# Kernel optimization log

Hardware: AMD Instinct MI355X
Metric: run time of the kernel (lower is better)

The kernel has to match this reference:

```python
import jax, jax.numpy as jnp
import numpy as np

U, I, E, D, R = 100000, 50000, 2000000, 64, 5


def setup_inputs() -> dict:
    key = jax.random.key(0)
    ks = jax.random.split(key, 14)
    def n(k, shape, scale=0.05):
        return jax.random.normal(k, shape, jnp.float32) * scale
    return {
        "user_feat": n(ks[0], (U, D), 1.0),
        "item_feat": n(ks[1], (I, D), 1.0),
        "rating_feat": n(ks[2], (R, D), 1.0),
        "row_idxs": jax.random.randint(ks[3], (E,), 0, I),   # item index per edge
        "col_idxs": jax.random.randint(ks[4], (E,), 0, U),   # user index per edge (dst)
        "rating": jax.random.randint(ks[5], (E,), 0, R),
        # gv = Linear(2D,D)+ReLU -> Linear(D,D)+ReLU
        "gv_w1": n(ks[6], (2 * D, D)), "gv_b1": jnp.zeros((D,), jnp.float32),
        "gv_w2": n(ks[7], (D, D)),     "gv_b2": jnp.zeros((D,), jnp.float32),
        # Attention: Linear(2D,D)+ReLU -> Linear(D,D)+ReLU -> Linear(D,1)
        "att_w1": n(ks[8], (2 * D, D)), "att_b1": jnp.zeros((D,), jnp.float32),
        "att_w2": n(ks[9], (D, D)),     "att_b2": jnp.zeros((D,), jnp.float32),
        "att_w3": n(ks[10], (D, 1)),    "att_b3": jnp.zeros((1,), jnp.float32),
        # output projection w = Linear(D,D)
        "w_w": n(ks[11], (D, D)), "w_b": jnp.zeros((D,), jnp.float32),
    }


def segment_softmax(logits, seg, num_segments):
    # numerically stable softmax over edges grouped by destination node
    m = jax.ops.segment_max(logits, seg, num_segments=num_segments)
    e = jnp.exp(logits - m[seg])
    s = jax.ops.segment_sum(e, seg, num_segments=num_segments)
    return e / s[seg]


def reference(user_feat, item_feat, rating_feat, row_idxs, col_idxs, rating,
              gv_w1, gv_b1, gv_w2, gv_b2,
              att_w1, att_b1, att_w2, att_b2, att_w3, att_b3,
              w_w, w_b):
    # gather per-edge embeddings
    r_emb = rating_feat[rating]          # [E, D]
    i_emb = item_feat[row_idxs]          # [E, D]
    u_emb = user_feat[col_idxs]          # [E, D]
    # gv MLP on concat(item, rating)
    x = jnp.concatenate([i_emb, r_emb], axis=1)              # [E, 2D]
    h1 = jax.nn.relu(x @ gv_w1 + gv_b1)
    x_ia = jax.nn.relu(h1 @ gv_w2 + gv_b2)                   # [E, D]
    # attention MLP on concat(x_ia, user)
    a = jnp.concatenate([x_ia, u_emb], axis=1)               # [E, 2D]
    a = jax.nn.relu(a @ att_w1 + att_b1)
    a = jax.nn.relu(a @ att_w2 + att_b2)
    weight = (a @ att_w3 + att_b3)[:, 0]                     # [E]
    # edge_softmax over incoming edges of each destination (user) node
    value = segment_softmax(weight, col_idxs, U)             # [E]
    # scatter-sum weighted messages to users
    h = jax.ops.segment_sum(x_ia * value[:, None], col_idxs, num_segments=U)  # [U, D]
    # act is None -> plain linear
    return h @ w_w + w_b
```

## Files before the change

### kernel.cpp

```cpp
#include <hip/hip_runtime.h>
#include <hip/hip_bf16.h>
#include <hip/hip_fp8.h>

#define U_N 100000
#define I_N 50000
#define E_N 2000000
#define R_N 5
#define C_N (I_N*R_N)
#define NBLK_U 391
#define NBLK_E 7813
#define NBLK_C 1954
#define NBUCKC 196

typedef __hip_bfloat16 bf16_t;
typedef unsigned short u16;
typedef unsigned char u8;
typedef __attribute__((ext_vector_type(8))) short bf16x8;
typedef __attribute__((ext_vector_type(4))) float f32x4;

__device__ __forceinline__ float blo(unsigned u){ return __uint_as_float(u<<16); }
__device__ __forceinline__ float bhi(unsigned u){ return __uint_as_float(u & 0xffff0000u); }
__device__ __forceinline__ unsigned pkbf(float a, float b){
  __hip_bfloat162 t = __float22bfloat162_rn(float2{a,b});
  union { __hip_bfloat162 h; unsigned u; } cv; cv.h = t; return cv.u;
}
__device__ __forceinline__ u16 f2b(float v){
  union { __hip_bfloat16 h; u16 u; } cv; cv.h = __float2bfloat16(v); return cv.u;
}
__device__ __forceinline__ float f8f(unsigned b){
  __hip_fp8_e4m3 h; h.__x = (u8)b; return (float)h;
}
__device__ __forceinline__ unsigned ff8(float f){
  __hip_fp8_e4m3 h(f); return (unsigned)h.__x;
}

__global__ __launch_bounds__(256) void k_histQ(const int* __restrict__ cols, int* __restrict__ hist_g){
  __shared__ int histI[NBUCKC];
  int t = threadIdx.x, b = blockIdx.x;
  if(t < NBUCKC) histI[t] = 0;
  __syncthreads();
  int e = b*256 + t;
  if(e < E_N) atomicAdd(&histI[cols[e] >> 9], 1);
  __syncthreads();
  if(t < NBUCKC) hist_g[(size_t)b*NBUCKC + t] = histI[t];
}

__global__ __launch_bounds__(256) void k_scanQ(const int* __restrict__ hist_g, int* __restrict__ boff_g,
                                               int* __restrict__ qtot){
  __shared__ int wsum[4];
  int t = threadIdx.x, q = blockIdx.x;
  int lane = t & 63, wv = t >> 6;
  int running = 0;
  for(int c0=0; c0<NBLK_E; c0+=256){
    int b = c0 + t;
    int v = (b < NBLK_E) ? hist_g[(size_t)b*NBUCKC + q] : 0;
    int inc = v;
#pragma unroll
    for(int off=1; off<64; off<<=1){
      int x = __shfl(inc, lane-off);
      if(lane >= off) inc += x;
    }
    if(lane == 63) wsum[wv] = inc;
    __syncthreads();
    int w0=wsum[0], w1=wsum[1], w2=wsum[2], w3=wsum[3];
    int wpre = (wv>0?w0:0) + (wv>1?w1:0) + (wv>2?w2:0);
    if(b < NBLK_E) boff_g[(size_t)b*NBUCKC + q] = running + wpre + inc - v;
    running += w0 + w1 + w2 + w3;
    __syncthreads();
  }
  if(t == 0) qtot[q] = running;
}

__global__ void k_scanT(const int* __restrict__ qtot, int* __restrict__ qbase){
  __shared__ int s[256];
  int t = threadIdx.x;
  int v = (t < NBUCKC) ? qtot[t] : 0;
  s[t] = v; __syncthreads();
  for(int off=1; off<256; off<<=1){
    int x = (t>=off) ? s[t-off] : 0;
    __syncthreads();
    s[t] += x;
    __syncthreads();
  }
  if(t < NBUCKC) qbase[t] = s[t] - v;
  if(t == 255)   qbase[NBUCKC] = s[255];
}

__global__ __launch_bounds__(256) void k_place2(const int* __restrict__ rows, const int* __restrict__ cols,
                                                const int* __restrict__ rats,
                                                const int* __restrict__ boff_g, const int* __restrict__ qbase,
                                                unsigned* __restrict__ uc2){
  __shared__ int rankI[NBUCKC];
  __shared__ int baseI[NBUCKC];
  int t = threadIdx.x, b = blockIdx.x;
  if(t < NBUCKC){
    rankI[t] = 0;
    baseI[t] = qbase[t] + boff_g[(size_t)b*NBUCKC + t];
  }
  __syncthreads();
  int e = b*256 + t;
  if(e < E_N){
    int u = cols[e];
    int c = rows[e]*5 + rats[e];
    int q = u >> 9;
    int r = atomicAdd(&rankI[q], 1);
    uc2[baseI[q] + r] = ((unsigned)(u & 511) << 18) | (unsigned)c;
  }
}

__global__ __launch_bounds__(256) void k_fineB1(const unsigned* __restrict__ uc2, const int* __restrict__ qbase,
                                                int* __restrict__ cnt){
  __shared__ int hist[512];
  int t = threadIdx.x, q = blockIdx.x;
  hist[t] = 0; hist[t+256] = 0;
  __syncthreads();
  int r0 = qbase[q], r1 = qbase[q+1];
  for(int j=r0+t; j<r1; j+=256) atomicAdd(&hist[(uc2[j]>>18) & 511], 1);
  __syncthreads();
  cnt[q*512 + t]       = hist[t];
  cnt[q*512 + t + 256] = hist[t+256];
}

__global__ __launch_bounds__(256) void k_scanA(const int* __restrict__ cnt, int* __restrict__ start,
                                               int* __restrict__ bsum){
  __shared__ int s[256];
  int t = threadIdx.x, i = blockIdx.x*256 + t;
  int v = (i < U_N) ? cnt[i] : 0;
  s[t] = v; __syncthreads();
  for(int off=1; off<256; off<<=1){
    int x = (t>=off) ? s[t-off] : 0;
    __syncthreads();
    s[t] += x;
    __syncthreads();
  }
  start[i] = s[t] - v;
  if(t == 255) bsum[blockIdx.x] = s[255];
}

__global__ void k_scanB(int* bsum, int n){
  __shared__ int s[512];
  int t = threadIdx.x;
  int v = (t < n) ? bsum[t] : 0;
  s[t] = v; __syncthreads();
  for(int off=1; off<512; off<<=1){
    int x = (t>=off) ? s[t-off] : 0;
    __syncthreads();
    s[t] += x;
    __syncthreads();
  }
  if(t < n) bsum[t] = s[t] - v;
}

__global__ __launch_bounds__(256) void k_scanC(int* start, const int* __restrict__ bsum){
  int i = blockIdx.x*256 + threadIdx.x;
  start[i] += bsum[blockIdx.x];
}

__global__ __launch_bounds__(256) void k_fineB2(const unsigned* __restrict__ uc2, const int* __restrict__ qbase,
                                                const int* __restrict__ start,
                                                int* __restrict__ u_s, int* __restrict__ c_s){
  __shared__ int fillb[512];
  __shared__ int startb[512];
  int t = threadIdx.x, q = blockIdx.x;
  fillb[t] = 0; fillb[t+256] = 0;
  startb[t]     = start[q*512 + t];
  startb[t+256] = start[q*512 + t + 256];
  __syncthreads();
  int r0 = qbase[q], r1 = qbase[q+1];
  for(int j=r0+t; j<r1; j+=256){
    unsigned v = uc2[j];
    int ul = (int)((v>>18) & 511);
    int off = atomicAdd(&fillb[ul], 1);
    int pos = startb[ul] + off;
    u_s[pos] = (q<<9) | ul;
    c_s[pos] = (int)(v & 0x3FFFFu);
  }
}

__global__ void k_ratpart(const float* __restrict__ rf, const float* __restrict__ w1,
                          const float* __restrict__ b1, float* __restrict__ out){
  int t = threadIdx.x; if(t >= R_N*64) return;
  int r = t>>6, d = t&63;
  float acc = b1[d];
  for(int k=0;k<64;k++) acc += rf[r*64 + k] * w1[(64+k)*64 + d];
  out[t] = acc;
}

__global__ __launch_bounds__(256) void k_prepw6(const float* __restrict__ w1, const float* __restrict__ a1,
                                                const float* __restrict__ w2, const float* __restrict__ a2,
                                                const float* __restrict__ ww,
                                                u16* w1t, u16* u1t, u16* w2t, u16* a1t, u16* a2t, u16* wwt){
  int idx = (blockIdx.x & 15)*256 + threadIdx.x;
  int sec = blockIdx.x >> 4;
  int d = idx >> 6, k = idx & 63;
  const float* src; u16* dst; int ko = 0;
  switch(sec){
    case 0: src=w1; dst=w1t; break;
    case 1: src=a1; dst=u1t; ko=64; break;
    case 2: src=w2; dst=w2t; break;
    case 3: src=a1; dst=a1t; break;
    case 4: src=a2; dst=a2t; break;
    default: src=ww; dst=wwt; break;
  }
  dst[idx] = f2b(src[(size_t)(ko+k)*64 + d]);
}

template<bool BIAS>
__global__ __launch_bounds__(256) void k_rowgemm(const float4* __restrict__ in,
                                                 const uint4* __restrict__ wt,
                                                 const float* __restrict__ bias,
                                                 uint4* __restrict__ outp, int n){
  __shared__ uint4 A_u4[2048];
  __shared__ uint4 W_u4[512];
  __shared__ float bsh[64];
  u16* A16 = (u16*)A_u4;
  const int tid = threadIdx.x;
  for(int cid = tid; cid < 512; cid += 256){
    int dd = cid >> 3, ch = cid & 7;
    W_u4[dd*8 + (ch ^ (dd&7))] = wt[cid];
  }
  if(BIAS && tid < 64) bsh[tid] = bias[tid];
  const int base = blockIdx.x*256;
  const int ch = tid & 7;
#pragma unroll
  for(int it=0; it<8; ++it){
    int s = it*32 + (tid>>3);
    int r = base + s;
    uint4 o = {0,0,0,0};
    if(r < n){
      const float4* p = in + (size_t)r*16 + ch*2;
      float4 v0 = p[0], v1 = p[1];
      o.x = pkbf(v0.x, v0.y); o.y = pkbf(v0.z, v0.w);
      o.z = pkbf(v1.x, v1.y); o.w = pkbf(v1.z, v1.w);
    }
    A_u4[s*8 + (ch ^ (s&7))] = o;
  }
  __syncthreads();
  const int l = tid & 63, w = tid >> 6;
  const int lr = l & 15, g = l >> 4;
  bf16x8 bfr[4][2];
#pragma unroll
  for(int nt=0; nt<4; ++nt)
#pragma unroll
    for(int kk=0; kk<2; ++kk){
      int d = nt*16 + lr;
      bfr[nt][kk] = *(const bf16x8*)&W_u4[d*8 + ((kk*4+g) ^ (d&7))];
    }
  float bv[4];
#pragma unroll
  for(int nt=0; nt<4; ++nt) bv[nt] = BIAS ? bsh[nt*16 + lr] : 0.f;
#pragma unroll
  for(int t=0; t<4; ++t){
    int s = w*64 + t*16 + lr;
    bf16x8 af0 = *(const bf16x8*)&A_u4[s*8 + ((0*4+g) ^ (s&7))];
    bf16x8 af1 = *(const bf16x8*)&A_u4[s*8 + ((1*4+g) ^ (s&7))];
    f32x4 acc[4];
#pragma unroll
    for(int nt=0; nt<4; ++nt){
      f32x4 c0 = { bv[nt], bv[nt], bv[nt], bv[nt] };
      c0 = __builtin_amdgcn_mfma_f32_16x16x32_bf16(af0, bfr[nt][0], c0, 0, 0, 0);
      c0 = __builtin_amdgcn_mfma_f32_16x16x32_bf16(af1, bfr[nt][1], c0, 0, 0, 0);
      acc[nt] = c0;
    }
#pragma unroll
    for(int nt=0; nt<4; ++nt){
      int d = nt*16 + lr;
#pragma unroll
      for(int reg=0; reg<4; ++reg){
        int srow = w*64 + t*16 + g*4 + reg;
        A16[srow*64 + ((d>>3)^(srow&7))*8 + (d&7)] = f2b(acc[nt][reg]);
      }
    }
  }
#pragma unroll
  for(int it=0; it<8; ++it){
    int s = w*64 + it*8 + (l>>3);
    int c2 = l & 7;
    int r = base + s;
    if(r < n) outp[(size_t)r*8 + c2] = A_u4[s*8 + (c2 ^ (s&7))];
  }
}

__global__ __launch_bounds__(256) void k_combo_mfma(const uint4* __restrict__ itemp,
                                                    const float4* __restrict__ ratp,
                                                    const uint4* __restrict__ w2t_g, const uint4* __restrict__ a1t_g,
                                                    const uint4* __restrict__ wwt_g,
                                                    const float* __restrict__ b2,
                                                    uint4* __restrict__ y_o, u8* __restrict__ xa1_o8){
  __shared__ uint4 A_u4[1024];
  __shared__ uint4 X_u4[1024];
  __shared__ uint4 W2_u4[512];
  __shared__ uint4 A1_u4[512];
  __shared__ uint4 WW_u4[512];
  __shared__ float4 rsh4[80];
  __shared__ float b2sh[64];
  u16* A16 = (u16*)A_u4;
  u16* X16 = (u16*)X_u4;
  const int tid = threadIdx.x;
  for(int cid = tid; cid < 512; cid += 256){
    int dd = cid >> 3, ch = cid & 7;
    W2_u4[dd*8 + (ch ^ (dd&7))] = w2t_g[cid];
    A1_u4[dd*8 + (ch ^ (dd&7))] = a1t_g[cid];
    WW_u4[dd*8 + (ch ^ (dd&7))] = wwt_g[cid];
  }
  if(tid < 80) rsh4[tid] = ratp[tid];
  if(tid < 64) b2sh[tid] = b2[tid];
  __syncthreads();

  const int base = blockIdx.x*128;
  const int ch = tid & 7;
#pragma unroll
  for(int it=0; it<4; ++it){
    int s = it*32 + (tid>>3);
    int cidx = base + s;
    uint4 o = {0,0,0,0};
    if(cidx < C_N){
      int i = cidx/5, r = cidx - i*5;
      uint4 iv = itemp[(size_t)i*8 + ch];
      float4 r0 = rsh4[r*16 + ch*2], r1 = rsh4[r*16 + ch*2 + 1];
      o.x = pkbf(fmaxf(blo(iv.x)+r0.x,0.f), fmaxf(bhi(iv.x)+r0.y,0.f));
      o.y = pkbf(fmaxf(blo(iv.y)+r0.z,0.f), fmaxf(bhi(iv.y)+r0.w,0.f));
      o.z = pkbf(fmaxf(blo(iv.z)+r1.x,0.f), fmaxf(bhi(iv.z)+r1.y,0.f));
      o.w = pkbf(fmaxf(blo(iv.w)+r1.z,0.f), fmaxf(bhi(iv.w)+r1.w,0.f));
    }
    A_u4[s*8 + (ch ^ (s&7))] = o;
  }
  __syncthreads();

  const int l = tid & 63, w = tid >> 6;
  const int lr = l & 15, g = l >> 4;
  bf16x8 w2f[4][2], a1f[4][2], wwf[4][2];
#pragma unroll
  for(int nt=0; nt<4; ++nt)
#pragma unroll
    for(int kk=0; kk<2; ++kk){
      int d = nt*16 + lr;
      w2f[nt][kk] = *(const bf16x8*)&W2_u4[d*8 + ((kk*4+g) ^ (d&7))];
      a1f[nt][kk] = *(const bf16x8*)&A1_u4[d*8 + ((kk*4+g) ^ (d&7))];
      wwf[nt][kk] = *(const bf16x8*)&WW_u4[d*8 + ((kk*4+g) ^ (d&7))];
    }
  float b2v[4];
#pragma unroll
  for(int nt=0; nt<4; ++nt) b2v[nt] = b2sh[nt*16 + lr];

#pragma unroll
  for(int t=0; t<2; ++t){
    int s = w*32 + t*16 + lr;
    bf16x8 af0 = *(const bf16x8*)&A_u4[s*8 + ((0*4+g) ^ (s&7))];
    bf16x8 af1 = *(const bf16x8*)&A_u4[s*8 + ((1*4+g) ^ (s&7))];
#pragma unroll
    for(int nt=0; nt<4; ++nt){
      f32x4 c0 = { b2v[nt], b2v[nt], b2v[nt], b2v[nt] };
      c0 = __builtin_amdgcn_mfma_f32_16x16x32_bf16(af0, w2f[nt][0], c0, 0, 0, 0);
      c0 = __builtin_amdgcn_mfma_f32_16x16x32_bf16(af1, w2f[nt][1], c0, 0, 0, 0);
      int d = nt*16 + lr;
#pragma unroll
      for(int reg=0; reg<4; ++reg){
        int srow = w*32 + t*16 + g*4 + reg;
        X16[srow*64 + ((d>>3)^(srow&7))*8 + (d&7)] = f2b(fmaxf(c0[reg], 0.f));
      }
    }
    bf16x8 xf0 = *(const bf16x8*)&X_u4[s*8 + ((0*4+g) ^ (s&7))];
    bf16x8 xf1 = *(const bf16x8*)&X_u4[s*8 + ((1*4+g) ^ (s&7))];
#pragma unroll
    for(int nt=0; nt<4; ++nt){
      f32x4 c0 = { 0.f, 0.f, 0.f, 0.f };
      c0 = __builtin_amdgcn_mfma_f32_16x16x32_bf16(xf0, a1f[nt][0], c0, 0, 0, 0);
      c0 = __builtin_amdgcn_mfma_f32_16x16x32_bf16(xf1, a1f[nt][1], c0, 0, 0, 0);
      int d = nt*16 + lr;
#pragma unroll
      for(int reg=0; reg<4; ++reg){
        int srow = w*32 + t*16 + g*4 + reg;
        A16[srow*64 + ((d>>3)^(srow&7))*8 + (d&7)] = f2b(c0[reg]);
      }
    }
#pragma unroll
    for(int nt=0; nt<4; ++nt){
      f32x4 c0 = { 0.f, 0.f, 0.f, 0.f };
      c0 = __builtin_amdgcn_mfma_f32_16x16x32_bf16(xf0, wwf[nt][0], c0, 0, 0, 0);
      c0 = __builtin_amdgcn_mfma_f32_16x16x32_bf16(xf1, wwf[nt][1], c0, 0, 0, 0);
      int d = nt*16 + lr;
#pragma unroll
      for(int reg=0; reg<4; ++reg){
        int srow = w*32 + t*16 + g*4 + reg;
        X16[srow*64 + ((d>>3)^(srow&7))*8 + (d&7)] = f2b(c0[reg]);
      }
    }
  }
#pragma unroll
  for(int it=0; it<4; ++it){
    int s = w*32 + it*8 + (l>>3);
    int c2 = l & 7;
    int r = base + s;
    if(r < C_N) y_o[(size_t)r*8 + c2] = X_u4[s*8 + (c2 ^ (s&7))];
  }
#pragma unroll
  for(int it=0; it<2; ++it){
    int slot = it*64 + l;
    int rl = slot >> 2;
    int c4 = slot & 3;
    int s = w*32 + rl;
    int r = base + s;
    if(r < C_N){
      uint4 h0 = A_u4[s*8 + ((c4*2+0) ^ (s&7))];
      uint4 h1 = A_u4[s*8 + ((c4*2+1) ^ (s&7))];
      uint4 o;
      o.x = ff8(blo(h0.x)) | (ff8(bhi(h0.x))<<8) | (ff8(blo(h0.y))<<16) | (ff8(bhi(h0.y))<<24);
      o.y = ff8(blo(h0.z)) | (ff8(bhi(h0.z))<<8) | (ff8(blo(h0.w))<<16) | (ff8(bhi(h0.w))<<24);
      o.z = ff8(blo(h1.x)) | (ff8(bhi(h1.x))<<8) | (ff8(blo(h1.y))<<16) | (ff8(bhi(h1.y))<<24);
      o.w = ff8(blo(h1.z)) | (ff8(bhi(h1.z))<<8) | (ff8(blo(h1.w))<<16) | (ff8(bhi(h1.w))<<24);
      *(uint4*)(xa1_o8 + (size_t)r*64 + c4*16) = o;
    }
  }
}

__global__ __launch_bounds__(256) void k_edge_mfma(const int* __restrict__ u_s, const int* __restrict__ c_s,
                                                   const u8* __restrict__ xa1p8, const uint4* __restrict__ userp,
                                                   const u16* __restrict__ w2t_g,
                                                   const float* __restrict__ a2b,
                                                   const float* __restrict__ a3w, const float* __restrict__ a3b,
                                                   float* __restrict__ wlog){
  const int tid = threadIdx.x;
  const int base = blockIdx.x*256;
  const int l = tid & 63, w = tid >> 6;
  const int lr = l & 15;
  const int g  = l >> 4;
  bf16x8 bf[4][2];
#pragma unroll
  for(int nt=0; nt<4; ++nt)
#pragma unroll
    for(int kk=0; kk<2; ++kk){
      int d = nt*16 + lr;
      bf[nt][kk] = *(const bf16x8*)(w2t_g + d*64 + kk*32 + g*8);
    }
  float b2v[4], a3v[4];
#pragma unroll
  for(int nt=0; nt<4; ++nt){ b2v[nt] = a2b[nt*16 + lr]; a3v[nt] = a3w[nt*16 + lr]; }
  const float a3b0 = a3b[0];

  int cin[4], uin[4];
#pragma unroll
  for(int t=0; t<4; ++t){
    int s = base + w*64 + t*16 + lr;
    cin[t] = (s < E_N) ? c_s[s] : 0;
    uin[t] = (s < E_N) ? u_s[s] : 0;
  }
  uint2 xq0 = *(const uint2*)(xa1p8 + (size_t)cin[0]*64 + g*8);
  uint2 xq1 = *(const uint2*)(xa1p8 + (size_t)cin[0]*64 + 32 + g*8);
  uint4 uv0 = userp[(size_t)uin[0]*8 + g];
  uint4 uv1 = userp[(size_t)uin[0]*8 + 4 + g];

#pragma unroll
  for(int t=0; t<4; ++t){
    uint2 nx0, nx1; uint4 nu0, nu1;
    if(t < 3){
      nx0 = *(const uint2*)(xa1p8 + (size_t)cin[t+1]*64 + g*8);
      nx1 = *(const uint2*)(xa1p8 + (size_t)cin[t+1]*64 + 32 + g*8);
      nu0 = userp[(size_t)uin[t+1]*8 + g];
      nu1 = userp[(size_t)uin[t+1]*8 + 4 + g];
    }
    union { uint4 u4; bf16x8 v; } a0, a1;
    a0.u4.x = pkbf(fmaxf(f8f(xq0.x&255u)+blo(uv0.x),0.f),       fmaxf(f8f((xq0.x>>8)&255u)+bhi(uv0.x),0.f));
    a0.u4.y = pkbf(fmaxf(f8f((xq0.x>>16)&255u)+blo(uv0.y),0.f), fmaxf(f8f(xq0.x>>24)+bhi(uv0.y),0.f));
    a0.u4.z = pkbf(fmaxf(f8f(xq0.y&255u)+blo(uv0.z),0.f),       fmaxf(f8f((xq0.y>>8)&255u)+bhi(uv0.z),0.f));
    a0.u4.w = pkbf(fmaxf(f8f((xq0.y>>16)&255u)+blo(uv0.w),0.f), fmaxf(f8f(xq0.y>>24)+bhi(uv0.w),0.f));
    a1.u4.x = pkbf(fmaxf(f8f(xq1.x&255u)+blo(uv1.x),0.f),       fmaxf(f8f((xq1.x>>8)&255u)+bhi(uv1.x),0.f));
    a1.u4.y = pkbf(fmaxf(f8f((xq1.x>>16)&255u)+blo(uv1.y),0.f), fmaxf(f8f(xq1.x>>24)+bhi(uv1.y),0.f));
    a1.u4.z = pkbf(fmaxf(f8f(xq1.y&255u)+blo(uv1.z),0.f),       fmaxf(f8f((xq1.y>>8)&255u)+bhi(uv1.z),0.f));
    a1.u4.w = pkbf(fmaxf(f8f((xq1.y>>16)&255u)+blo(uv1.w),0.f), fmaxf(f8f(xq1.y>>24)+bhi(uv1.w),0.f));
    f32x4 acc[4];
#pragma unroll
    for(int nt=0; nt<4; ++nt){
      f32x4 c0 = { b2v[nt], b2v[nt], b2v[nt], b2v[nt] };
      c0 = __builtin_amdgcn_mfma_f32_16x16x32_bf16(a0.v, bf[nt][0], c0, 0, 0, 0);
      c0 = __builtin_amdgcn_mfma_f32_16x16x32_bf16(a1.v, bf[nt][1], c0, 0, 0, 0);
      acc[nt] = c0;
    }
    float s0=0.f, s1=0.f, s2=0.f, s3=0.f;
#pragma unroll
    for(int nt=0; nt<4; ++nt){
      s0 += fmaxf(acc[nt][0], 0.f) * a3v[nt];
      s1 += fmaxf(acc[nt][1], 0.f) * a3v[nt];
      s2 += fmaxf(acc[nt][2], 0.f) * a3v[nt];
      s3 += fmaxf(acc[nt][3], 0.f) * a3v[nt];
    }
#pragma unroll
    for(int mask=1; mask<16; mask<<=1){
      s0 += __shfl_xor(s0, mask);
      s1 += __shfl_xor(s1, mask);
      s2 += __shfl_xor(s2, mask);
      s3 += __shfl_xor(s3, mask);
    }
    if(lr == 0){
      int e0 = base + w*64 + t*16 + g*4;
      if(e0+0 < E_N) wlog[e0+0] = s0 + a3b0;
      if(e0+1 < E_N) wlog[e0+1] = s1 + a3b0;
      if(e0+2 < E_N) wlog[e0+2] = s2 + a3b0;
      if(e0+3 < E_N) wlog[e0+3] = s3 + a3b0;
    }
    xq0 = nx0; xq1 = nx1; uv0 = nu0; uv1 = nu1;
  }
}

__global__ __launch_bounds__(256) void k_aggf(const int* __restrict__ start,
                                              const int* __restrict__ u_s, const int* __restrict__ c_s,
                                              const float* __restrict__ wlog,
                                              const u16* __restrict__ Y,
                                              const float* __restrict__ wb,
                                              float* __restrict__ out){
  __shared__ uint4 Ysh[4][256];
  int w = threadIdx.x >> 6, l = threadIdx.x & 63;
  int lr = l & 15, g = l >> 4;
  int base = (blockIdx.x*4 + w) * 16;
  if(base >= U_N) return;
  int s0g = start[base];
  int s1g = start[base+16];
  int myu = base + lr;
  int sA = s0g & ~31;
  int nch = (s1g - sA + 31) >> 5;
  const int kb = g*8;

  float m = -1e30f;
  for(int ch=0; ch<nch; ++ch){
    int e0 = sA + ch*32;
    float4 wv0 = *(const float4*)(wlog + e0 + kb);
    float4 wv1 = *(const float4*)(wlog + e0 + kb + 4);
    int4 u0 = *(const int4*)(u_s + e0 + kb);
    int4 u1 = *(const int4*)(u_s + e0 + kb + 4);
    if(u0.x==myu) m = fmaxf(m, wv0.x);
    if(u0.y==myu) m = fmaxf(m, wv0.y);
    if(u0.z==myu) m = fmaxf(m, wv0.z);
    if(u0.w==myu) m = fmaxf(m, wv0.w);
    if(u1.x==myu) m = fmaxf(m, wv1.x);
    if(u1.y==myu) m = fmaxf(m, wv1.y);
    if(u1.z==myu) m = fmaxf(m, wv1.z);
    if(u1.w==myu) m = fmaxf(m, wv1.w);
  }
  m = fmaxf(m, __shfl_xor(m, 16));
  m = fmaxf(m, __shfl_xor(m, 32));

  f32x4 acc[4];
#pragma unroll
  for(int nt=0; nt<4; ++nt) acc[nt] = f32x4{0.f,0.f,0.f,0.f};
  float ssum = 0.f;
  u16* Ysh16 = (u16*)&Ysh[w][0];
  for(int ch=0; ch<nch; ++ch){
    int e0 = sA + ch*32;
    int rowe = e0 + (l>>1);
    int crow = c_s[rowe];
    const uint4* yp = (const uint4*)Y + (size_t)crow*8 + (l&1)*4;
    uint4* dst = &Ysh[w][(l>>1)*8 + (l&1)*4];
    dst[0] = yp[0]; dst[1] = yp[1]; dst[2] = yp[2]; dst[3] = yp[3];

    float4 wv0 = *(const float4*)(wlog + e0 + kb);
    float4 wv1 = *(const float4*)(wlog + e0 + kb + 4);
    int4 u0 = *(const int4*)(u_s + e0 + kb);
    int4 u1 = *(const int4*)(u_s + e0 + kb + 4);
    bf16x8 af;
    {
      bool mt; float e;
      mt = (u0.x==myu); e = __expf((mt?wv0.x:-1e30f) - m); ssum += mt?e:0.f; af[0] = mt?(short)f2b(e):(short)0;
      mt = (u0.y==myu); e = __expf((mt?wv0.y:-1e30f) - m); ssum += mt?e:0.f; af[1] = mt?(short)f2b(e):(short)0;
      mt = (u0.z==myu); e = __expf((mt?wv0.z:-1e30f) - m); ssum += mt?e:0.f; af[2] = mt?(short)f2b(e):(short)0;
      mt = (u0.w==myu); e = __expf((mt?wv0.w:-1e30f) - m); ssum += mt?e:0.f; af[3] = mt?(short)f2b(e):(short)0;
      mt = (u1.x==myu); e = __expf((mt?wv1.x:-1e30f) - m); ssum += mt?e:0.f; af[4] = mt?(short)f2b(e):(short)0;
      mt = (u1.y==myu); e = __expf((mt?wv1.y:-1e30f) - m); ssum += mt?e:0.f; af[5] = mt?(short)f2b(e):(short)0;
      mt = (u1.z==myu); e = __expf((mt?wv1.z:-1e30f) - m); ssum += mt?e:0.f; af[6] = mt?(short)f2b(e):(short)0;
      mt = (u1.w==myu); e = __expf((mt?wv1.w:-1e30f) - m); ssum += mt?e:0.f; af[7] = mt?(short)f2b(e):(short)0;
    }
    bf16x8 b0, b1, b2, b3;
#pragma unroll
    for(int j=0; j<8; ++j){
      int r = (kb + j)*64 + lr;
      b0[j] = (short)Ysh16[r];
      b1[j] = (short)Ysh16[r+16];
      b2[j] = (short)Ysh16[r+32];
      b3[j] = (short)Ysh16[r+48];
    }
    acc[0] = __builtin_amdgcn_mfma_f32_16x16x32_bf16(af, b0, acc[0], 0, 0, 0);
    acc[1] = __builtin_amdgcn_mfma_f32_16x16x32_bf16(af, b1, acc[1], 0, 0, 0);
    acc[2] = __builtin_amdgcn_mfma_f32_16x16x32_bf16(af, b2, acc[2], 0, 0, 0);
    acc[3] = __builtin_amdgcn_mfma_f32_16x16x32_bf16(af, b3, acc[3], 0, 0, 0);
  }
  ssum += __shfl_xor(ssum, 16);
  ssum += __shfl_xor(ssum, 32);
  float inv = (ssum > 0.f) ? (1.f/ssum) : 0.f;
  float wbv[4];
#pragma unroll
  for(int nt=0; nt<4; ++nt) wbv[nt] = wb[nt*16 + lr];
#pragma unroll
  for(int reg=0; reg<4; ++reg){
    float sc = __shfl(inv, g*4 + reg);
    int u = base + g*4 + reg;
#pragma unroll
    for(int nt=0; nt<4; ++nt)
      out[(size_t)u*64 + nt*16 + lr] = acc[nt][reg]*sc + wbv[nt];
  }
}

extern "C" void kernel_launch(void* const* d_in, const int* in_sizes, int n_in,
                              void* d_out, int out_size, void* d_ws, size_t ws_size,
                              hipStream_t stream){
  (void)in_sizes; (void)n_in; (void)out_size; (void)ws_size;
  const float4* user_feat  = (const float4*)d_in[0];
  const float4* item_feat  = (const float4*)d_in[1];
  const float*  rating_feat= (const float*)d_in[2];
  const int*    rows       = (const int*)d_in[3];
  const int*    cols       = (const int*)d_in[4];
  const int*    rats       = (const int*)d_in[5];
  const float* gv_w1 = (const float*)d_in[6];
  const float* gv_b1 = (const float*)d_in[7];
  const float* gv_w2 = (const float*)d_in[8];
  const float* gv_b2 = (const float*)d_in[9];
  const float* att_w1= (const float*)d_in[10];
  const float* att_b1= (const float*)d_in[11];
  const float* att_w2= (const float*)d_in[12];
  const float* att_b2= (const float*)d_in[13];
  const float* att_w3= (const float*)d_in[14];
  const float* att_b3= (const float*)d_in[15];
  const float* w_w   = (const float*)d_in[16];
  const float* w_b   = (const float*)d_in[17];
  float* out = (float*)d_out;

  char* ws = (char*)d_ws; size_t off = 0;
  auto take = [&](size_t b)->char*{ char* p = ws + off; off = (off + b + 255) & ~(size_t)255; return p; };
  bf16_t*   item_part  = (bf16_t*)take((size_t)I_N*64*2);
  bf16_t*   user_part  = (bf16_t*)take((size_t)U_N*64*2);
  float*    rating_part= (float*) take((size_t)R_N*64*4);
  bf16_t*   y_t        = (bf16_t*)take((size_t)C_N*64*2);
  u8*       xa1_8      = (u8*)    take((size_t)C_N*64);
  float*    wlog_s     = (float*) take((size_t)E_N*4);
  int*      c_s        = (int*)   take((size_t)E_N*4);
  int*      u_s        = (int*)   take((size_t)E_N*4);
  unsigned* uc2        = (unsigned*)take((size_t)E_N*4);
  int*      hist_g     = (int*)   take((size_t)NBLK_E*NBUCKC*4);
  int*      boff_g     = (int*)   take((size_t)NBLK_E*NBUCKC*4);
  int*      qtot       = (int*)   take((size_t)256*4);
  int*      qbase      = (int*)   take((size_t)256*4);
  int*      cnt        = (int*)   take((size_t)(NBUCKC*512+256)*4);
  int*      start      = (int*)   take((size_t)(NBUCKC*512+256)*4);
  int*      bsum       = (int*)   take((size_t)512*4);
  u16*      w1t        = (u16*)   take((size_t)4096*2);
  u16*      u1t        = (u16*)   take((size_t)4096*2);
  u16*      w2t        = (u16*)   take((size_t)4096*2);
  u16*      a1t        = (u16*)   take((size_t)4096*2);
  u16*      a2t        = (u16*)   take((size_t)4096*2);
  u16*      wwt        = (u16*)   take((size_t)4096*2);

  k_histQ <<<NBLK_E, 256, 0, stream>>>(cols, hist_g);
  k_scanQ <<<NBUCKC, 256, 0, stream>>>(hist_g, boff_g, qtot);
  k_scanT <<<1, 256, 0, stream>>>(qtot, qbase);
  k_place2<<<NBLK_E, 256, 0, stream>>>(rows, cols, rats, boff_g, qbase, uc2);
  k_fineB1<<<NBUCKC, 256, 0, stream>>>(uc2, qbase, cnt);
  k_scanA <<<NBLK_U, 256, 0, stream>>>(cnt, start, bsum);
  k_scanB <<<1, 512, 0, stream>>>(bsum, NBLK_U);
  k_scanC <<<NBLK_U, 256, 0, stream>>>(start, bsum);
  k_fineB2<<<NBUCKC, 256, 0, stream>>>(uc2, qbase, start, u_s, c_s);
  k_ratpart <<<1, 320, 0, stream>>>(rating_feat, gv_w1, gv_b1, rating_part);
  k_prepw6  <<<96, 256, 0, stream>>>(gv_w1, att_w1, gv_w2, att_w2, w_w, w1t, u1t, w2t, a1t, a2t, wwt);
  k_rowgemm<false><<<(I_N+255)/256, 256, 0, stream>>>(item_feat, (const uint4*)w1t, nullptr,
                                                      (uint4*)item_part, I_N);
  k_rowgemm<true> <<<NBLK_U, 256, 0, stream>>>(user_feat, (const uint4*)u1t, att_b1,
                                               (uint4*)user_part, U_N);
  k_combo_mfma<<<NBLK_C, 256, 0, stream>>>((const uint4*)item_part, (const float4*)rating_part,
                                           (const uint4*)w2t, (const uint4*)a1t, (const uint4*)wwt, gv_b2,
                                           (uint4*)y_t, xa1_8);
  k_edge_mfma<<<NBLK_E, 256, 0, stream>>>(u_s, c_s, xa1_8, (const uint4*)user_part,
                                          w2t, att_b2, att_w3, att_b3, wlog_s);
  k_aggf <<<(U_N/64)+1, 256, 0, stream>>>(start, u_s, c_s, wlog_s, (const u16*)y_t, w_b, out);
}
```

Baseline: 310.5 us.

## Pack user/item indices into one sorted word and double-buffer aggregation loads

Replaces the separate sorted user and item index arrays with a single packed 32-bit array. It stores 14 bits of user id above an 18-bit combo id, which cuts index write and read traffic in the sort, edge and aggregation kernels. The edge kernel rebuilds the full user id from a per-block bucket lookup plus a short scan over bucket boundaries, and its gathers are restructured into a two-deep prefetch. The aggregation kernel double-buffers the gathered Y rows in shared memory so the next chunk's loads overlap the current MFMAs. The cost is an extra small kernel, more shared memory, and a per-edge while loop over bucket boundaries.

```diff
diff --git a/kernel.cpp b/kernel.cpp
--- a/kernel.cpp
+++ b/kernel.cpp
@@ -86,6 +86,14 @@
   if(t == 255)   qbase[NBUCKC] = s[255];
 }
 
+__global__ __launch_bounds__(256) void k_blockq(const int* __restrict__ qbase, int* __restrict__ blockq){
+  int b = blockIdx.x*256 + threadIdx.x; if(b >= NBLK_E) return;
+  int e = b*256;
+  int lo = 0, hi = NBUCKC-1;
+  while(lo < hi){ int mid = (lo+hi+1)>>1; if(qbase[mid] <= e) lo = mid; else hi = mid-1; }
+  blockq[b] = lo;
+}
+
 __global__ __launch_bounds__(256) void k_place2(const int* __restrict__ rows, const int* __restrict__ cols,
                                                 const int* __restrict__ rats,
                                                 const int* __restrict__ boff_g, const int* __restrict__ qbase,
@@ -104,7 +112,7 @@
     int c = rows[e]*5 + rats[e];
     int q = u >> 9;
     int r = atomicAdd(&rankI[q], 1);
-    uc2[baseI[q] + r] = ((unsigned)(u & 511) << 18) | (unsigned)c;
+    uc2[baseI[q] + r] = ((unsigned)(u & 16383) << 18) | (unsigned)c;
   }
 }
 
@@ -158,7 +166,7 @@
 
 __global__ __launch_bounds__(256) void k_fineB2(const unsigned* __restrict__ uc2, const int* __restrict__ qbase,
                                                 const int* __restrict__ start,
-                                                int* __restrict__ u_s, int* __restrict__ c_s){
+                                                unsigned* __restrict__ uc3){
   __shared__ int fillb[512];
   __shared__ int startb[512];
   int t = threadIdx.x, q = blockIdx.x;
@@ -171,9 +179,7 @@
     unsigned v = uc2[j];
     int ul = (int)((v>>18) & 511);
     int off = atomicAdd(&fillb[ul], 1);
-    int pos = startb[ul] + off;
-    u_s[pos] = (q<<9) | ul;
-    c_s[pos] = (int)(v & 0x3FFFFu);
+    uc3[startb[ul] + off] = v;
   }
 }
 
@@ -414,7 +420,8 @@
   }
 }
 
-__global__ __launch_bounds__(256) void k_edge_mfma(const int* __restrict__ u_s, const int* __restrict__ c_s,
+__global__ __launch_bounds__(256) void k_edge_mfma(const unsigned* __restrict__ uc3,
+                                                   const int* __restrict__ qbase, const int* __restrict__ blockq,
                                                    const u8* __restrict__ xa1p8, const uint4* __restrict__ userp,
                                                    const u16* __restrict__ w2t_g,
                                                    const float* __restrict__ a2b,
@@ -439,26 +446,19 @@
   const float a3b0 = a3b[0];
 
   int cin[4], uin[4];
+  int bq = blockq[blockIdx.x];
 #pragma unroll
   for(int t=0; t<4; ++t){
     int s = base + w*64 + t*16 + lr;
-    cin[t] = (s < E_N) ? c_s[s] : 0;
-    uin[t] = (s < E_N) ? u_s[s] : 0;
-  }
-  uint2 xq0 = *(const uint2*)(xa1p8 + (size_t)cin[0]*64 + g*8);
-  uint2 xq1 = *(const uint2*)(xa1p8 + (size_t)cin[0]*64 + 32 + g*8);
-  uint4 uv0 = userp[(size_t)uin[0]*8 + g];
-  uint4 uv1 = userp[(size_t)uin[0]*8 + 4 + g];
-
-#pragma unroll
-  for(int t=0; t<4; ++t){
-    uint2 nx0, nx1; uint4 nu0, nu1;
-    if(t < 3){
-      nx0 = *(const uint2*)(xa1p8 + (size_t)cin[t+1]*64 + g*8);
-      nx1 = *(const uint2*)(xa1p8 + (size_t)cin[t+1]*64 + 32 + g*8);
-      nu0 = userp[(size_t)uin[t+1]*8 + g];
-      nu1 = userp[(size_t)uin[t+1]*8 + 4 + g];
-    }
+    int sc = (s < E_N) ? s : (E_N-1);
+    unsigned vv = (s < E_N) ? uc3[s] : 0u;
+    int q = bq;
+    while(sc >= qbase[q+1]) ++q;
+    cin[t] = (int)(vv & 0x3FFFFu);
+    uin[t] = (q<<9) | (int)((vv>>18) & 511u);
+  }
+
+  auto compute = [&](uint2 xq0, uint2 xq1, uint4 uv0, uint4 uv1, int t){
     union { uint4 u4; bf16x8 v; } a0, a1;
     a0.u4.x = pkbf(fmaxf(f8f(xq0.x&255u)+blo(uv0.x),0.f),       fmaxf(f8f((xq0.x>>8)&255u)+bhi(uv0.x),0.f));
     a0.u4.y = pkbf(fmaxf(f8f((xq0.x>>16)&255u)+blo(uv0.y),0.f), fmaxf(f8f(xq0.x>>24)+bhi(uv0.y),0.f));
@@ -498,24 +498,45 @@
       if(e0+2 < E_N) wlog[e0+2] = s2 + a3b0;
       if(e0+3 < E_N) wlog[e0+3] = s3 + a3b0;
     }
-    xq0 = nx0; xq1 = nx1; uv0 = nu0; uv1 = nu1;
-  }
+  };
+
+  uint2 xA0 = *(const uint2*)(xa1p8 + (size_t)cin[0]*64 + g*8);
+  uint2 xA1 = *(const uint2*)(xa1p8 + (size_t)cin[0]*64 + 32 + g*8);
+  uint4 uA0 = userp[(size_t)uin[0]*8 + g];
+  uint4 uA1 = userp[(size_t)uin[0]*8 + 4 + g];
+  uint2 xB0 = *(const uint2*)(xa1p8 + (size_t)cin[1]*64 + g*8);
+  uint2 xB1 = *(const uint2*)(xa1p8 + (size_t)cin[1]*64 + 32 + g*8);
+  uint4 uB0 = userp[(size_t)uin[1]*8 + g];
+  uint4 uB1 = userp[(size_t)uin[1]*8 + 4 + g];
+
+  compute(xA0, xA1, uA0, uA1, 0);
+  xA0 = *(const uint2*)(xa1p8 + (size_t)cin[2]*64 + g*8);
+  xA1 = *(const uint2*)(xa1p8 + (size_t)cin[2]*64 + 32 + g*8);
+  uA0 = userp[(size_t)uin[2]*8 + g];
+  uA1 = userp[(size_t)uin[2]*8 + 4 + g];
+  compute(xB0, xB1, uB0, uB1, 1);
+  xB0 = *(const uint2*)(xa1p8 + (size_t)cin[3]*64 + g*8);
+  xB1 = *(const uint2*)(xa1p8 + (size_t)cin[3]*64 + 32 + g*8);
+  uB0 = userp[(size_t)uin[3]*8 + g];
+  uB1 = userp[(size_t)uin[3]*8 + 4 + g];
+  compute(xA0, xA1, uA0, uA1, 2);
+  compute(xB0, xB1, uB0, uB1, 3);
 }
 
 __global__ __launch_bounds__(256) void k_aggf(const int* __restrict__ start,
-                                              const int* __restrict__ u_s, const int* __restrict__ c_s,
+                                              const unsigned* __restrict__ uc3,
                                               const float* __restrict__ wlog,
                                               const u16* __restrict__ Y,
                                               const float* __restrict__ wb,
                                               float* __restrict__ out){
-  __shared__ uint4 Ysh[4][256];
+  __shared__ uint4 Ysh[2][4][256];
   int w = threadIdx.x >> 6, l = threadIdx.x & 63;
   int lr = l & 15, g = l >> 4;
   int base = (blockIdx.x*4 + w) * 16;
   if(base >= U_N) return;
   int s0g = start[base];
   int s1g = start[base+16];
-  int myu = base + lr;
+  unsigned ml = (unsigned)((base + lr) & 16383);
   int sA = s0g & ~31;
   int nch = (s1g - sA + 31) >> 5;
   const int kb = g*8;
@@ -525,16 +546,16 @@
     int e0 = sA + ch*32;
     float4 wv0 = *(const float4*)(wlog + e0 + kb);
     float4 wv1 = *(const float4*)(wlog + e0 + kb + 4);
-    int4 u0 = *(const int4*)(u_s + e0 + kb);
-    int4 u1 = *(const int4*)(u_s + e0 + kb + 4);
-    if(u0.x==myu) m = fmaxf(m, wv0.x);
-    if(u0.y==myu) m = fmaxf(m, wv0.y);
-    if(u0.z==myu) m = fmaxf(m, wv0.z);
-    if(u0.w==myu) m = fmaxf(m, wv0.w);
-    if(u1.x==myu) m = fmaxf(m, wv1.x);
-    if(u1.y==myu) m = fmaxf(m, wv1.y);
-    if(u1.z==myu) m = fmaxf(m, wv1.z);
-    if(u1.w==myu) m = fmaxf(m, wv1.w);
+    uint4 v0 = *(const uint4*)(uc3 + e0 + kb);
+    uint4 v1 = *(const uint4*)(uc3 + e0 + kb + 4);
+    if((v0.x>>18)==ml) m = fmaxf(m, wv0.x);
+    if((v0.y>>18)==ml) m = fmaxf(m, wv0.y);
+    if((v0.z>>18)==ml) m = fmaxf(m, wv0.z);
+    if((v0.w>>18)==ml) m = fmaxf(m, wv0.w);
+    if((v1.x>>18)==ml) m = fmaxf(m, wv1.x);
+    if((v1.y>>18)==ml) m = fmaxf(m, wv1.y);
+    if((v1.z>>18)==ml) m = fmaxf(m, wv1.z);
+    if((v1.w>>18)==ml) m = fmaxf(m, wv1.w);
   }
   m = fmaxf(m, __shfl_xor(m, 16));
   m = fmaxf(m, __shfl_xor(m, 32));
@@ -543,31 +564,42 @@
 #pragma unroll
   for(int nt=0; nt<4; ++nt) acc[nt] = f32x4{0.f,0.f,0.f,0.f};
   float ssum = 0.f;
-  u16* Ysh16 = (u16*)&Ysh[w][0];
+  int buf = 0;
+  if(nch > 0){
+    int rowe = sA + (l>>1);
+    int crow = (int)(uc3[rowe] & 0x3FFFFu);
+    const uint4* yp = (const uint4*)Y + (size_t)crow*8 + (l&1)*4;
+    uint4 y0=yp[0], y1=yp[1], y2=yp[2], y3=yp[3];
+    uint4* dst = &Ysh[0][w][(l>>1)*8 + (l&1)*4];
+    dst[0]=y0; dst[1]=y1; dst[2]=y2; dst[3]=y3;
+  }
   for(int ch=0; ch<nch; ++ch){
     int e0 = sA + ch*32;
-    int rowe = e0 + (l>>1);
-    int crow = c_s[rowe];
-    const uint4* yp = (const uint4*)Y + (size_t)crow*8 + (l&1)*4;
-    uint4* dst = &Ysh[w][(l>>1)*8 + (l&1)*4];
-    dst[0] = yp[0]; dst[1] = yp[1]; dst[2] = yp[2]; dst[3] = yp[3];
-
+    uint4 n0, n1, n2, n3;
+    bool hasNext = (ch+1 < nch);
+    if(hasNext){
+      int rowe = e0 + 32 + (l>>1);
+      int crowN = (int)(uc3[rowe] & 0x3FFFFu);
+      const uint4* yp = (const uint4*)Y + (size_t)crowN*8 + (l&1)*4;
+      n0=yp[0]; n1=yp[1]; n2=yp[2]; n3=yp[3];
+    }
     float4 wv0 = *(const float4*)(wlog + e0 + kb);
     float4 wv1 = *(const float4*)(wlog + e0 + kb + 4);
-    int4 u0 = *(const int4*)(u_s + e0 + kb);
-    int4 u1 = *(const int4*)(u_s + e0 + kb + 4);
+    uint4 v0 = *(const uint4*)(uc3 + e0 + kb);
+    uint4 v1 = *(const uint4*)(uc3 + e0 + kb + 4);
     bf16x8 af;
     {
       bool mt; float e;
-      mt = (u0.x==myu); e = __expf((mt?wv0.x:-1e30f) - m); ssum += mt?e:0.f; af[0] = mt?(short)f2b(e):(short)0;
-      mt = (u0.y==myu); e = __expf((mt?wv0.y:-1e30f) - m); ssum += mt?e:0.f; af[1] = mt?(short)f2b(e):(short)0;
-      mt = (u0.z==myu); e = __expf((mt?wv0.z:-1e30f) - m); ssum += mt?e:0.f; af[2] = mt?(short)f2b(e):(short)0;
-      mt = (u0.w==myu); e = __expf((mt?wv0.w:-1e30f) - m); ssum += mt?e:0.f; af[3] = mt?(short)f2b(e):(short)0;
-      mt = (u1.x==myu); e = __expf((mt?wv1.x:-1e30f) - m); ssum += mt?e:0.f; af[4] = mt?(short)f2b(e):(short)0;
-      mt = (u1.y==myu); e = __expf((mt?wv1.y:-1e30f) - m); ssum += mt?e:0.f; af[5] = mt?(short)f2b(e):(short)0;
-      mt = (u1.z==myu); e = __expf((mt?wv1.z:-1e30f) - m); ssum += mt?e:0.f; af[6] = mt?(short)f2b(e):(short)0;
-      mt = (u1.w==myu); e = __expf((mt?wv1.w:-1e30f) - m); ssum += mt?e:0.f; af[7] = mt?(short)f2b(e):(short)0;
-    }
+      mt = ((v0.x>>18)==ml); e = __expf((mt?wv0.x:-1e30f) - m); ssum += mt?e:0.f; af[0] = mt?(short)f2b(e):(short)0;
+      mt = ((v0.y>>18)==ml); e = __expf((mt?wv0.y:-1e30f) - m); ssum += mt?e:0.f; af[1] = mt?(short)f2b(e):(short)0;
+      mt = ((v0.z>>18)==ml); e = __expf((mt?wv0.z:-1e30f) - m); ssum += mt?e:0.f; af[2] = mt?(short)f2b(e):(short)0;
+      mt = ((v0.w>>18)==ml); e = __expf((mt?wv0.w:-1e30f) - m); ssum += mt?e:0.f; af[3] = mt?(short)f2b(e):(short)0;
+      mt = ((v1.x>>18)==ml); e = __expf((mt?wv1.x:-1e30f) - m); ssum += mt?e:0.f; af[4] = mt?(short)f2b(e):(short)0;
+      mt = ((v1.y>>18)==ml); e = __expf((mt?wv1.y:-1e30f) - m); ssum += mt?e:0.f; af[5] = mt?(short)f2b(e):(short)0;
+      mt = ((v1.z>>18)==ml); e = __expf((mt?wv1.z:-1e30f) - m); ssum += mt?e:0.f; af[6] = mt?(short)f2b(e):(short)0;
+      mt = ((v1.w>>18)==ml); e = __expf((mt?wv1.w:-1e30f) - m); ssum += mt?e:0.f; af[7] = mt?(short)f2b(e):(short)0;
+    }
+    u16* Ysh16 = (u16*)&Ysh[buf][w][0];
     bf16x8 b0, b1, b2, b3;
 #pragma unroll
     for(int j=0; j<8; ++j){
@@ -581,6 +613,11 @@
     acc[1] = __builtin_amdgcn_mfma_f32_16x16x32_bf16(af, b1, acc[1], 0, 0, 0);
     acc[2] = __builtin_amdgcn_mfma_f32_16x16x32_bf16(af, b2, acc[2], 0, 0, 0);
     acc[3] = __builtin_amdgcn_mfma_f32_16x16x32_bf16(af, b3, acc[3], 0, 0, 0);
+    if(hasNext){
+      uint4* dst = &Ysh[buf^1][w][(l>>1)*8 + (l&1)*4];
+      dst[0]=n0; dst[1]=n1; dst[2]=n2; dst[3]=n3;
+    }
+    buf ^= 1;
   }
   ssum += __shfl_xor(ssum, 16);
   ssum += __shfl_xor(ssum, 32);
@@ -630,13 +667,13 @@
   bf16_t*   y_t        = (bf16_t*)take((size_t)C_N*64*2);
   u8*       xa1_8      = (u8*)    take((size_t)C_N*64);
   float*    wlog_s     = (float*) take((size_t)E_N*4);
-  int*      c_s        = (int*)   take((size_t)E_N*4);
-  int*      u_s        = (int*)   take((size_t)E_N*4);
+  unsigned* uc3        = (unsigned*)take((size_t)E_N*4);
   unsigned* uc2        = (unsigned*)take((size_t)E_N*4);
   int*      hist_g     = (int*)   take((size_t)NBLK_E*NBUCKC*4);
   int*      boff_g     = (int*)   take((size_t)NBLK_E*NBUCKC*4);
   int*      qtot       = (int*)   take((size_t)256*4);
   int*      qbase      = (int*)   take((size_t)256*4);
+  int*      blockq     = (int*)   take((size_t)NBLK_E*4);
   int*      cnt        = (int*)   take((size_t)(NBUCKC*512+256)*4);
   int*      start      = (int*)   take((size_t)(NBUCKC*512+256)*4);
   int*      bsum       = (int*)   take((size_t)512*4);
@@ -650,12 +687,13 @@
   k_histQ <<<NBLK_E, 256, 0, stream>>>(cols, hist_g);
   k_scanQ <<<NBUCKC, 256, 0, stream>>>(hist_g, boff_g, qtot);
   k_scanT <<<1, 256, 0, stream>>>(qtot, qbase);
+  k_blockq<<<(NBLK_E+255)/256, 256, 0, stream>>>(qbase, blockq);
   k_place2<<<NBLK_E, 256, 0, stream>>>(rows, cols, rats, boff_g, qbase, uc2);
   k_fineB1<<<NBUCKC, 256, 0, stream>>>(uc2, qbase, cnt);
   k_scanA <<<NBLK_U, 256, 0, stream>>>(cnt, start, bsum);
   k_scanB <<<1, 512, 0, stream>>>(bsum, NBLK_U);
   k_scanC <<<NBLK_U, 256, 0, stream>>>(start, bsum);
-  k_fineB2<<<NBUCKC, 256, 0, stream>>>(uc2, qbase, start, u_s, c_s);
+  k_fineB2<<<NBUCKC, 256, 0, stream>>>(uc2, qbase, start, uc3);
   k_ratpart <<<1, 320, 0, stream>>>(rating_feat, gv_w1, gv_b1, rating_part);
   k_prepw6  <<<96, 256, 0, stream>>>(gv_w1, att_w1, gv_w2, att_w2, w_w, w1t, u1t, w2t, a1t, a2t, wwt);
   k_rowgemm<false><<<(I_N+255)/256, 256, 0, stream>>>(item_feat, (const uint4*)w1t, nullptr,
@@ -665,7 +703,7 @@
   k_combo_mfma<<<NBLK_C, 256, 0, stream>>>((const uint4*)item_part, (const float4*)rating_part,
                                            (const uint4*)w2t, (const uint4*)a1t, (const uint4*)wwt, gv_b2,
                                            (uint4*)y_t, xa1_8);
-  k_edge_mfma<<<NBLK_E, 256, 0, stream>>>(u_s, c_s, xa1_8, (const uint4*)user_part,
+  k_edge_mfma<<<NBLK_E, 256, 0, stream>>>(uc3, qbase, blockq, xa1_8, (const uint4*)user_part,
                                           w2t, att_b2, att_w3, att_b3, wlog_s);
-  k_aggf <<<(U_N/64)+1, 256, 0, stream>>>(start, u_s, c_s, wlog_s, (const u16*)y_t, w_b, out);
-}
+  k_aggf <<<(U_N/64)+1, 256, 0, stream>>>(start, uc3, wlog_s, (const u16*)y_t, w_b, out);
+}
```

Result: faster. 293.3 us (-5.5%).
